# Optimization experiments

Measured on AMD Instinct MI355X. Metric: run time of the kernel, lower is better.

## Reference

```python
import jax, jax.numpy as jnp
import numpy as np

N = 100000       # nodes
E = 1600000      # edges (before self-loops)
D_IN = 128       # input feature dim
HID = 16         # hidden channels per head
HEADS = 4
D_OUT = 32       # output communities
NEG_SLOPE = 0.2  # PyG GATConv default leaky_relu slope


def setup_inputs() -> dict:
    key = jax.random.key(0)
    ks = jax.random.split(key, 10)
    s = 0.1
    x = jax.random.normal(ks[0], (N, D_IN), jnp.float32)
    edge_index = jax.random.randint(ks[1], (2, E), 0, N, dtype=jnp.int64)
    W1 = jax.random.normal(ks[2], (D_IN, HEADS * HID), jnp.float32) * s
    a_src1 = jax.random.normal(ks[3], (HEADS, HID), jnp.float32) * s
    a_dst1 = jax.random.normal(ks[4], (HEADS, HID), jnp.float32) * s
    b1 = jnp.zeros((HEADS * HID,), jnp.float32)
    W2 = jax.random.normal(ks[5], (HEADS * HID, D_OUT), jnp.float32) * s
    a_src2 = jax.random.normal(ks[6], (1, D_OUT), jnp.float32) * s
    a_dst2 = jax.random.normal(ks[7], (1, D_OUT), jnp.float32) * s
    b2 = jnp.zeros((D_OUT,), jnp.float32)
    return {"x": x, "edge_index": edge_index, "W1": W1, "a_src1": a_src1,
            "a_dst1": a_dst1, "b1": b1, "W2": W2, "a_src2": a_src2,
            "a_dst2": a_dst2, "b2": b2}


def _segment_softmax(logits, seg, n):
    # softmax over edges grouped by destination node (per head)
    m = jax.ops.segment_max(logits, seg, num_segments=n)
    m = jnp.where(jnp.isfinite(m), m, 0.0)  # guard empty segments
    e = jnp.exp(logits - m[seg])
    z = jax.ops.segment_sum(e, seg, num_segments=n)
    return e / (z[seg] + 1e-16)


def _gat_conv(x, src, dst, W, a_src, a_dst, bias, heads, out_c, concat):
    n = x.shape[0]
    h = (x @ W).reshape(n, heads, out_c)                 # [N,H,C]
    al_s = jnp.einsum('nhc,hc->nh', h, a_src)            # [N,H]
    al_d = jnp.einsum('nhc,hc->nh', h, a_dst)            # [N,H]
    logits = jax.nn.leaky_relu(al_s[src] + al_d[dst], NEG_SLOPE)  # [E,H]
    alpha = _segment_softmax(logits, dst, n)             # [E,H]
    msg = h[src] * alpha[..., None]                      # [E,H,C]
    out = jax.ops.segment_sum(msg, dst, num_segments=n)  # [N,H,C]
    out = out.reshape(n, heads * out_c) if concat else out.mean(axis=1)
    return out + bias


def reference(x, edge_index, W1, a_src1, a_dst1, b1, W2, a_src2, a_dst2, b2):
    loops = jnp.arange(N, dtype=edge_index.dtype)
    src = jnp.concatenate([edge_index[0], loops])
    dst = jnp.concatenate([edge_index[1], loops])
    h = _gat_conv(x, src, dst, W1, a_src1, a_dst1, b1, HEADS, HID, True)
    h = jax.nn.elu(h)
    return _gat_conv(h, src, dst, W2, a_src2, a_dst2, b2, 1, D_OUT, False)
```

## Files before the change

### kernel.cpp

```cpp
#include <hip/hip_runtime.h>
#include <hip/hip_fp16.h>
#include <math.h>

#define NN 100000
#define EE 1600000
#define DIN 128
#define C1 64
#define C2 32
#define NEG 0.2f

#define NB 1024
#define BSH 7
#define EPB 4096

static __device__ __forceinline__ float leaky(float x) { return x > 0.f ? x : NEG * x; }


__global__ __launch_bounds__(256) void k_chist(const int* __restrict__ ei, int* __restrict__ bhist) {
    __shared__ int h[NB];
    int t = threadIdx.x;
    for (int i = t; i < NB; i += 256) h[i] = 0;
    __syncthreads();
    int e0 = blockIdx.x * EPB;
#pragma unroll
    for (int j = 0; j < 16; j++) {
        int e = e0 + t + 256 * j;
        if (e < EE) atomicAdd(&h[ei[EE + e] >> BSH], 1);
    }
    __syncthreads();
    for (int i = t; i < NB; i += 256) {
        int c = h[i];
        if (c) atomicAdd(&bhist[i], c);
    }
}

__global__ __launch_bounds__(256) void k_bscan(const int* __restrict__ bhist,
                                               int* __restrict__ gbase, int* __restrict__ gcur) {
    __shared__ int s[256];
    int t = threadIdx.x;
    int base = t * 4;
    int v[4];
    int run = 0;
#pragma unroll
    for (int j = 0; j < 4; j++) {
        v[j] = run;
        run += bhist[base + j];
    }
    int val = run;
    s[t] = val;
    __syncthreads();
    for (int off = 1; off < 256; off <<= 1) {
        int add = (t >= off) ? s[t - off] : 0;
        __syncthreads();
        val += add;
        s[t] = val;
        __syncthreads();
    }
    int texcl = val - run;
#pragma unroll
    for (int j = 0; j < 4; j++) {
        gbase[base + j] = texcl + v[j];
        gcur[base + j] = texcl + v[j];
    }
}

__global__ __launch_bounds__(256) void k_bin(const int* __restrict__ ei, int* __restrict__ gcur,
                                             int* __restrict__ binned) {
    __shared__ int h[NB];
    __shared__ int base[NB];
    int t = threadIdx.x;
    for (int i = t; i < NB; i += 256) h[i] = 0;
    __syncthreads();
    int e0 = blockIdx.x * EPB;
    int src[16], dst[16];
#pragma unroll
    for (int j = 0; j < 16; j++) {
        int e = e0 + t + 256 * j;
        if (e < EE) {
            src[j] = ei[e];
            dst[j] = ei[EE + e];
            atomicAdd(&h[dst[j] >> BSH], 1);
        } else
            dst[j] = -1;
    }
    __syncthreads();
    for (int i = t; i < NB; i += 256) {
        int c = h[i];
        if (c) base[i] = atomicAdd(&gcur[i], c);
        h[i] = 0;
    }
    __syncthreads();
#pragma unroll
    for (int j = 0; j < 16; j++) {
        if (dst[j] >= 0) {
            int b = dst[j] >> BSH;
            int r = atomicAdd(&h[b], 1);
            binned[base[b] + r] = (src[j] << 7) | (dst[j] & 127);
        }
    }
}

__global__ __launch_bounds__(256) void k_bsort(const int* __restrict__ binned,
                                               const int* __restrict__ gbase,
                                               const int* __restrict__ bhist,
                                               int* __restrict__ rs, int* __restrict__ deg,
                                               int* __restrict__ csr) {
    __shared__ int h[128], cur[128], sc[128];
    int b = blockIdx.x, t = threadIdx.x;
    if (t < 128) h[t] = 0;
    __syncthreads();
    int gb = gbase[b], cnt = bhist[b];
    for (int i = t; i < cnt; i += 256) atomicAdd(&h[binned[gb + i] & 127], 1);
    __syncthreads();
    if (t < 128) sc[t] = h[t];
    __syncthreads();
    for (int off = 1; off < 128; off <<= 1) {
        int add = 0;
        if (t < 128 && t >= off) add = sc[t - off];
        __syncthreads();
        if (t < 128) sc[t] += add;
        __syncthreads();
    }
    if (t < 128) {
        int node = b * 128 + t;
        int excl = sc[t] - h[t];
        if (node < NN) {
            rs[node] = gb + excl;
            deg[node] = h[t];
        }
        cur[t] = excl;
    }
    __syncthreads();
    for (int i = t; i < cnt; i += 256) {
        int e = binned[gb + i];
        int r = atomicAdd(&cur[e & 127], 1);
        csr[gb + r] = e >> 7;
    }
}

__global__ __launch_bounds__(256, 2) void k_gemm1(
    const float* __restrict__ x, const float* __restrict__ W1,
    const float* __restrict__ a_s, const float* __restrict__ a_d,
    __half* __restrict__ h1h, float* __restrict__ als, float* __restrict__ ald) {
    __shared__ float xs[64 * 128];
    __shared__ float wsh[128 * 64];
    int t = threadIdx.x;
    int base = blockIdx.x * 64;
    for (int i = t; i < 2048; i += 256) ((float4*)wsh)[i] = ((const float4*)W1)[i];
    int maxn = NN - base;
    if (maxn > 64) maxn = 64;
    for (int i = t; i < 2048; i += 256) {
        int flat = i * 4;
        int n = flat >> 7;
        if (n < maxn) *(float4*)&xs[flat] = *(const float4*)&x[(size_t)(base + n) * 128 + (flat & 127)];
    }
    __syncthreads();
    int w = t >> 6, c = t & 63;
    int nb = w * 16;
    float acc[16];
#pragma unroll
    for (int j = 0; j < 16; j++) acc[j] = 0.f;
    for (int k = 0; k < 128; k += 4) {
        float w0 = wsh[k * 64 + c], w1 = wsh[(k + 1) * 64 + c];
        float w2 = wsh[(k + 2) * 64 + c], w3 = wsh[(k + 3) * 64 + c];
#pragma unroll
        for (int j = 0; j < 16; j++) {
            float4 xv = *(float4*)&xs[(nb + j) * 128 + k];
            acc[j] = fmaf(xv.x, w0, acc[j]);
            acc[j] = fmaf(xv.y, w1, acc[j]);
            acc[j] = fmaf(xv.z, w2, acc[j]);
            acc[j] = fmaf(xv.w, w3, acc[j]);
        }
    }
    float s_a = a_s[c], d_a = a_d[c];
    int hd = c >> 4;
#pragma unroll
    for (int j = 0; j < 16; j++) {
        int n = base + nb + j;
        float v = acc[j];
        float vs = v * s_a, vd = v * d_a;
#pragma unroll
        for (int off = 1; off < 16; off <<= 1) {
            vs += __shfl_xor(vs, off, 64);
            vd += __shfl_xor(vd, off, 64);
        }
        if (n < NN) {
            h1h[(size_t)n * 64 + c] = __float2half(v);
            if ((c & 15) == 0) {
                als[n * 4 + hd] = vs;
                ald[n * 4 + hd] = vd;
            }
        }
    }
}

__global__ __launch_bounds__(256) void k_edge1(
    const int* __restrict__ csr, const int* __restrict__ rs, const int* __restrict__ deg,
    const __half* __restrict__ h1h, const float* __restrict__ als, const float* __restrict__ ald,
    const float* __restrict__ b1, const float* __restrict__ W2,
    const float* __restrict__ as2, const float* __restrict__ ad2,
    __half* __restrict__ h2h, float* __restrict__ als2, float* __restrict__ ald2) {
    __shared__ float wsh[64 * 32];
    __shared__ float xld[4][64];
    __shared__ float pp[4][64][4];
    __shared__ int ss[4][64];
    int t = threadIdx.x;
    for (int i = t; i < 512; i += 256) ((float4*)wsh)[i] = ((const float4*)W2)[i];
    int w = t >> 6, lane = t & 63;
    int n = blockIdx.x * 4 + w;
    float4 ad4 = *(const float4*)&ald[n * 4];
    float4 an4 = *(const float4*)&als[n * 4];
    float ls0 = leaky(an4.x + ad4.x), ls1 = leaky(an4.y + ad4.y);
    float ls2 = leaky(an4.z + ad4.z), ls3 = leaky(an4.w + ad4.w);
    const __half2* h1p = (const __half2*)h1h;
    int cc = lane & 31, eh = lane >> 5;
    int hd2 = cc >> 3;
    float z = 0.f, acc0 = 0.f, acc1 = 0.f;
    if (eh == 0) {
        float2 fs = __half22float2(h1p[n * 32 + cc]);
        z = 1.f;
        acc0 = fs.x;
        acc1 = fs.y;
    }
    int s0 = rs[n], d = deg[n];
    for (int i0 = 0; i0 < d; i0 += 64) {
        int e = i0 + lane;
        int src = 0;
        float4 a4 = make_float4(-1e30f, -1e30f, -1e30f, -1e30f);
        if (e < d) {
            src = csr[s0 + e];
            a4 = *(const float4*)&als[src * 4];
        }
        float p0 = __expf(leaky(a4.x + ad4.x) - ls0);
        float p1 = __expf(leaky(a4.y + ad4.y) - ls1);
        float p2 = __expf(leaky(a4.z + ad4.z) - ls2);
        float p3 = __expf(leaky(a4.w + ad4.w) - ls3);
        ss[w][lane] = src;
        *(float4*)&pp[w][lane][0] = make_float4(p0, p1, p2, p3);
        int cnt = d - i0;
        if (cnt > 64) cnt = 64;
        int i = eh;
        for (; i + 6 < cnt; i += 8) {
            int sA = ss[w][i], sB = ss[w][i + 2], sC = ss[w][i + 4], sD = ss[w][i + 6];
            float pA = pp[w][i][hd2], pB = pp[w][i + 2][hd2];
            float pC = pp[w][i + 4][hd2], pD = pp[w][i + 6][hd2];
            float2 fA = __half22float2(h1p[sA * 32 + cc]);
            float2 fB = __half22float2(h1p[sB * 32 + cc]);
            float2 fC = __half22float2(h1p[sC * 32 + cc]);
            float2 fD = __half22float2(h1p[sD * 32 + cc]);
            z += (pA + pB) + (pC + pD);
            acc0 = fmaf(pA, fA.x, acc0);
            acc1 = fmaf(pA, fA.y, acc1);
            acc0 = fmaf(pB, fB.x, acc0);
            acc1 = fmaf(pB, fB.y, acc1);
            acc0 = fmaf(pC, fC.x, acc0);
            acc1 = fmaf(pC, fC.y, acc1);
            acc0 = fmaf(pD, fD.x, acc0);
            acc1 = fmaf(pD, fD.y, acc1);
        }
        for (; i < cnt; i += 2) {
            int sA = ss[w][i];
            float pA = pp[w][i][hd2];
            float2 f = __half22float2(h1p[sA * 32 + cc]);
            z += pA;
            acc0 = fmaf(pA, f.x, acc0);
            acc1 = fmaf(pA, f.y, acc1);
        }
    }
    acc0 += __shfl_xor(acc0, 32, 64);
    acc1 += __shfl_xor(acc1, 32, 64);
    z += __shfl_xor(z, 32, 64);
    float zi = __frcp_rn(z + 1e-16f);
    float o0 = acc0 * zi + b1[2 * cc];
    float o1 = acc1 * zi + b1[2 * cc + 1];
    float xv0 = o0 > 0.f ? o0 : expm1f(o0);
    float xv1 = o1 > 0.f ? o1 : expm1f(o1);
    if (eh == 0) {
        xld[w][2 * cc] = xv0;
        xld[w][2 * cc + 1] = xv1;
    }
    __syncthreads();

    int hi = lane >> 5, c2 = lane & 31;
    float accn = 0.f;
#pragma unroll
    for (int k = 0; k < 32; k++) {
        float xk = xld[w][hi * 32 + k];
        accn = fmaf(xk, wsh[(hi * 32 + k) * 32 + c2], accn);
    }
    accn += __shfl_xor(accn, 32, 64);
    float vs = accn * as2[c2], vd = accn * ad2[c2];
#pragma unroll
    for (int off = 1; off < 32; off <<= 1) {
        vs += __shfl_xor(vs, off, 64);
        vd += __shfl_xor(vd, off, 64);
    }
    if (lane < 32) h2h[(size_t)n * 32 + lane] = __float2half(accn);
    if (lane == 0) {
        als2[n] = vs;
        ald2[n] = vd;
    }
}

__global__ __launch_bounds__(256) void k_edge2(
    const int* __restrict__ csr, const int* __restrict__ rs, const int* __restrict__ deg,
    const __half* __restrict__ h2h, const float* __restrict__ als, const float* __restrict__ ald,
    const float* __restrict__ b2, float* __restrict__ out) {
    __shared__ float2 pst[4][64];
    int t = threadIdx.x;
    int w = t >> 6, lane = t & 63;
    int n = blockIdx.x * 4 + w;
    int cc = lane & 15, eq = lane >> 4;
    float ad = ald[n];
    float lself = leaky(als[n] + ad);
    const __half2* h2p = (const __half2*)h2h;
    float z = 0.f, acc0 = 0.f, acc1 = 0.f;
    if (eq == 0) {
        float2 fs = __half22float2(h2p[n * 16 + cc]);
        z = 1.f;
        acc0 = fs.x;
        acc1 = fs.y;
    }
    int s0 = rs[n], d = deg[n];
    for (int i0 = 0; i0 < d; i0 += 64) {
        int e = i0 + lane;
        int src = 0;
        float av = -1e30f;
        if (e < d) {
            src = csr[s0 + e];
            av = als[src];
        }
        float p = __expf(leaky(av + ad) - lself);
        pst[w][lane] = make_float2(__int_as_float(src), p);
        int cnt = d - i0;
        if (cnt > 64) cnt = 64;
        int i = eq;
        for (; i + 12 < cnt; i += 16) {
            float2 qA = pst[w][i], qB = pst[w][i + 4], qC = pst[w][i + 8], qD = pst[w][i + 12];
            int sA = __float_as_int(qA.x), sB = __float_as_int(qB.x);
            int sC = __float_as_int(qC.x), sD = __float_as_int(qD.x);
            float2 fA = __half22float2(h2p[sA * 16 + cc]);
            float2 fB = __half22float2(h2p[sB * 16 + cc]);
            float2 fC = __half22float2(h2p[sC * 16 + cc]);
            float2 fD = __half22float2(h2p[sD * 16 + cc]);
            z += (qA.y + qB.y) + (qC.y + qD.y);
            acc0 = fmaf(qA.y, fA.x, acc0);
            acc1 = fmaf(qA.y, fA.y, acc1);
            acc0 = fmaf(qB.y, fB.x, acc0);
            acc1 = fmaf(qB.y, fB.y, acc1);
            acc0 = fmaf(qC.y, fC.x, acc0);
            acc1 = fmaf(qC.y, fC.y, acc1);
            acc0 = fmaf(qD.y, fD.x, acc0);
            acc1 = fmaf(qD.y, fD.y, acc1);
        }
        for (; i < cnt; i += 4) {
            float2 q = pst[w][i];
            int sA = __float_as_int(q.x);
            float pA = q.y;
            float2 f = __half22float2(h2p[sA * 16 + cc]);
            z += pA;
            acc0 = fmaf(pA, f.x, acc0);
            acc1 = fmaf(pA, f.y, acc1);
        }
    }
    acc0 += __shfl_xor(acc0, 16, 64);
    acc0 += __shfl_xor(acc0, 32, 64);
    acc1 += __shfl_xor(acc1, 16, 64);
    acc1 += __shfl_xor(acc1, 32, 64);
    z += __shfl_xor(z, 16, 64);
    z += __shfl_xor(z, 32, 64);
    if (eq == 0) {
        float zi = __frcp_rn(z + 1e-16f);
        float o0 = acc0 * zi + b2[2 * cc];
        float o1 = acc1 * zi + b2[2 * cc + 1];
        *(float2*)&out[(size_t)n * 32 + 2 * cc] = make_float2(o0, o1);
    }
}

extern "C" void kernel_launch(void* const* d_in, const int* in_sizes, int n_in,
                              void* d_out, int out_size, void* d_ws, size_t ws_size,
                              hipStream_t stream) {
    const float* x = (const float*)d_in[0];
    const int* ei = (const int*)d_in[1];
    const float* W1 = (const float*)d_in[2];
    const float* as1 = (const float*)d_in[3];
    const float* ad1 = (const float*)d_in[4];
    const float* b1 = (const float*)d_in[5];
    const float* W2 = (const float*)d_in[6];
    const float* as2 = (const float*)d_in[7];
    const float* ad2 = (const float*)d_in[8];
    const float* b2 = (const float*)d_in[9];
    float* out = (float*)d_out;

    char* p = (char*)d_ws;
    auto alloc = [&](size_t bytes) -> char* {
        char* r = p;
        p += (bytes + 255) & ~(size_t)255;
        return r;
    };
    int* csr = (int*)alloc((size_t)EE * 4);
    int* rs = (int*)alloc((size_t)NN * 4);
    int* deg = (int*)alloc((size_t)NN * 4);
    int* bhist = (int*)alloc(NB * 4);
    int* gbase = (int*)alloc(NB * 4);
    int* gcur = (int*)alloc(NB * 4);
    __half* h1h = (__half*)alloc((size_t)NN * C1 * 2);
    float* als1 = (float*)alloc((size_t)NN * 4 * 4);
    float* ald1 = (float*)alloc((size_t)NN * 4 * 4);
    char* regionX = alloc((size_t)NN * C2 * 2 + (size_t)NN * 8 + 512);
    int* binned = (int*)regionX;
    __half* h2h = (__half*)regionX;
    float* als2 = (float*)(regionX + (size_t)NN * C2 * 2);
    float* ald2 = (float*)(regionX + (size_t)NN * C2 * 2 + (size_t)NN * 4);
    (void)ws_size;

    hipMemsetAsync(bhist, 0, NB * 4, stream);

    int nbin = (EE + EPB - 1) / EPB;
    k_chist<<<nbin, 256, 0, stream>>>(ei, bhist);
    k_bscan<<<1, 256, 0, stream>>>(bhist, gbase, gcur);
    k_bin<<<nbin, 256, 0, stream>>>(ei, gcur, binned);
    k_bsort<<<(NN + 127) / 128, 256, 0, stream>>>(binned, gbase, bhist, rs, deg, csr);

    k_gemm1<<<(NN + 63) / 64, 256, 0, stream>>>(x, W1, as1, ad1, h1h, als1, ald1);
    k_edge1<<<NN / 4, 256, 0, stream>>>(csr, rs, deg, h1h, als1, ald1, b1, W2, as2, ad2,
                                        h2h, als2, ald2);
    k_edge2<<<NN / 4, 256, 0, stream>>>(csr, rs, deg, h2h, als2, ald2, b2, out);
}
```

Before: 340.8 us.

## Fuse GEMM1 with histogram, vectorize edge binning, restructure edge1 LDS layout

Merges the layer-1 GEMM and the destination histogram into one launch, with extra blocks doing histogram work so the two independent stages overlap. Edge index loads in the histogram and binning kernels become int4 vector loads. k_edge1 stores per-head (src, weight) pairs in a padded LDS array, adds an 8-way unrolled gather loop, and raises the occupancy hint on both edge kernels. It also switches leaky_relu to fmaxf and ELU to __expf-1, which trades a little accuracy near zero for speed.

```diff
diff --git a/kernel.cpp b/kernel.cpp
--- a/kernel.cpp
+++ b/kernel.cpp
@@ -12,27 +12,92 @@
 #define NB 1024
 #define BSH 7
 #define EPB 4096
-
-static __device__ __forceinline__ float leaky(float x) { return x > 0.f ? x : NEG * x; }
-
-
-__global__ __launch_bounds__(256) void k_chist(const int* __restrict__ ei, int* __restrict__ bhist) {
-    __shared__ int h[NB];
+#define NGEMM 1563
+#define NCHIST 391
+
+static __device__ __forceinline__ float leaky(float x) { return fmaxf(x, NEG * x); }
+
+__global__ __launch_bounds__(256, 2) void k_gemm1_chist(
+    const float* __restrict__ x, const float* __restrict__ W1,
+    const float* __restrict__ a_s, const float* __restrict__ a_d,
+    __half* __restrict__ h1h, float* __restrict__ als, float* __restrict__ ald,
+    const int* __restrict__ ei, int* __restrict__ bhist) {
+    __shared__ float xs[64 * 128];
+    __shared__ float wsh[128 * 64];
     int t = threadIdx.x;
-    for (int i = t; i < NB; i += 256) h[i] = 0;
-    __syncthreads();
-    int e0 = blockIdx.x * EPB;
+    if (blockIdx.x >= NGEMM) {
+        int* h = (int*)xs;
+        for (int i = t; i < NB; i += 256) h[i] = 0;
+        __syncthreads();
+        const int4* d4p = (const int4*)(ei + EE);
+        int i40 = (blockIdx.x - NGEMM) * (EPB / 4);
+#pragma unroll
+        for (int j = 0; j < 4; j++) {
+            int idx = i40 + t + 256 * j;
+            if (idx < EE / 4) {
+                int4 d4 = d4p[idx];
+                atomicAdd(&h[d4.x >> BSH], 1);
+                atomicAdd(&h[d4.y >> BSH], 1);
+                atomicAdd(&h[d4.z >> BSH], 1);
+                atomicAdd(&h[d4.w >> BSH], 1);
+            }
+        }
+        __syncthreads();
+        for (int i = t; i < NB; i += 256) {
+            int c = h[i];
+            if (c) atomicAdd(&bhist[i], c);
+        }
+        return;
+    }
+    int base = blockIdx.x * 64;
+    for (int i = t; i < 2048; i += 256) ((float4*)wsh)[i] = ((const float4*)W1)[i];
+    int maxn = NN - base;
+    if (maxn > 64) maxn = 64;
+    for (int i = t; i < 2048; i += 256) {
+        int flat = i * 4;
+        int n = flat >> 7;
+        if (n < maxn) *(float4*)&xs[flat] = *(const float4*)&x[(size_t)(base + n) * 128 + (flat & 127)];
+    }
+    __syncthreads();
+    int w = t >> 6, c = t & 63;
+    int nb = w * 16;
+    float acc[16];
+#pragma unroll
+    for (int j = 0; j < 16; j++) acc[j] = 0.f;
+    for (int k = 0; k < 128; k += 4) {
+        float w0 = wsh[k * 64 + c], w1 = wsh[(k + 1) * 64 + c];
+        float w2 = wsh[(k + 2) * 64 + c], w3 = wsh[(k + 3) * 64 + c];
+#pragma unroll
+        for (int j = 0; j < 16; j++) {
+            float4 xv = *(float4*)&xs[(nb + j) * 128 + k];
+            acc[j] = fmaf(xv.x, w0, acc[j]);
+            acc[j] = fmaf(xv.y, w1, acc[j]);
+            acc[j] = fmaf(xv.z, w2, acc[j]);
+            acc[j] = fmaf(xv.w, w3, acc[j]);
+        }
+    }
+    float s_a = a_s[c], d_a = a_d[c];
+    int hd = c >> 4;
 #pragma unroll
     for (int j = 0; j < 16; j++) {
-        int e = e0 + t + 256 * j;
-        if (e < EE) atomicAdd(&h[ei[EE + e] >> BSH], 1);
-    }
-    __syncthreads();
-    for (int i = t; i < NB; i += 256) {
-        int c = h[i];
-        if (c) atomicAdd(&bhist[i], c);
-    }
-}
+        int n = base + nb + j;
+        float v = acc[j];
+        float vs = v * s_a, vd = v * d_a;
+#pragma unroll
+        for (int off = 1; off < 16; off <<= 1) {
+            vs += __shfl_xor(vs, off, 64);
+            vd += __shfl_xor(vd, off, 64);
+        }
+        if (n < NN) {
+            h1h[(size_t)n * 64 + c] = __float2half(v);
+            if ((c & 15) == 0) {
+                als[n * 4 + hd] = vs;
+                ald[n * 4 + hd] = vd;
+            }
+        }
+    }
+}
+
 
 __global__ __launch_bounds__(256) void k_bscan(const int* __restrict__ bhist,
                                                int* __restrict__ gbase, int* __restrict__ gcur) {
@@ -71,17 +136,23 @@
     int t = threadIdx.x;
     for (int i = t; i < NB; i += 256) h[i] = 0;
     __syncthreads();
-    int e0 = blockIdx.x * EPB;
-    int src[16], dst[16];
-#pragma unroll
-    for (int j = 0; j < 16; j++) {
-        int e = e0 + t + 256 * j;
-        if (e < EE) {
-            src[j] = ei[e];
-            dst[j] = ei[EE + e];
-            atomicAdd(&h[dst[j] >> BSH], 1);
-        } else
-            dst[j] = -1;
+    const int4* s4p = (const int4*)ei;
+    const int4* d4p = (const int4*)(ei + EE);
+    int i40 = blockIdx.x * (EPB / 4);
+    int4 s4[4], d4[4];
+    bool val[4];
+#pragma unroll
+    for (int j = 0; j < 4; j++) {
+        int idx = i40 + t + 256 * j;
+        val[j] = idx < EE / 4;
+        if (val[j]) {
+            s4[j] = s4p[idx];
+            d4[j] = d4p[idx];
+            atomicAdd(&h[d4[j].x >> BSH], 1);
+            atomicAdd(&h[d4[j].y >> BSH], 1);
+            atomicAdd(&h[d4[j].z >> BSH], 1);
+            atomicAdd(&h[d4[j].w >> BSH], 1);
+        }
     }
     __syncthreads();
     for (int i = t; i < NB; i += 256) {
@@ -91,11 +162,16 @@
     }
     __syncthreads();
 #pragma unroll
-    for (int j = 0; j < 16; j++) {
-        if (dst[j] >= 0) {
-            int b = dst[j] >> BSH;
-            int r = atomicAdd(&h[b], 1);
-            binned[base[b] + r] = (src[j] << 7) | (dst[j] & 127);
+    for (int j = 0; j < 4; j++) {
+        if (val[j]) {
+            int ss[4] = {s4[j].x, s4[j].y, s4[j].z, s4[j].w};
+            int dd[4] = {d4[j].x, d4[j].y, d4[j].z, d4[j].w};
+#pragma unroll
+            for (int q = 0; q < 4; q++) {
+                int b = dd[q] >> BSH;
+                int r = atomicAdd(&h[b], 1);
+                binned[base[b] + r] = (ss[q] << 7) | (dd[q] & 127);
+            }
         }
     }
 }
@@ -138,63 +214,7 @@
     }
 }
 
-__global__ __launch_bounds__(256, 2) void k_gemm1(
-    const float* __restrict__ x, const float* __restrict__ W1,
-    const float* __restrict__ a_s, const float* __restrict__ a_d,
-    __half* __restrict__ h1h, float* __restrict__ als, float* __restrict__ ald) {
-    __shared__ float xs[64 * 128];
-    __shared__ float wsh[128 * 64];
-    int t = threadIdx.x;
-    int base = blockIdx.x * 64;
-    for (int i = t; i < 2048; i += 256) ((float4*)wsh)[i] = ((const float4*)W1)[i];
-    int maxn = NN - base;
-    if (maxn > 64) maxn = 64;
-    for (int i = t; i < 2048; i += 256) {
-        int flat = i * 4;
-        int n = flat >> 7;
-        if (n < maxn) *(float4*)&xs[flat] = *(const float4*)&x[(size_t)(base + n) * 128 + (flat & 127)];
-    }
-    __syncthreads();
-    int w = t >> 6, c = t & 63;
-    int nb = w * 16;
-    float acc[16];
-#pragma unroll
-    for (int j = 0; j < 16; j++) acc[j] = 0.f;
-    for (int k = 0; k < 128; k += 4) {
-        float w0 = wsh[k * 64 + c], w1 = wsh[(k + 1) * 64 + c];
-        float w2 = wsh[(k + 2) * 64 + c], w3 = wsh[(k + 3) * 64 + c];
-#pragma unroll
-        for (int j = 0; j < 16; j++) {
-            float4 xv = *(float4*)&xs[(nb + j) * 128 + k];
-            acc[j] = fmaf(xv.x, w0, acc[j]);
-            acc[j] = fmaf(xv.y, w1, acc[j]);
-            acc[j] = fmaf(xv.z, w2, acc[j]);
-            acc[j] = fmaf(xv.w, w3, acc[j]);
-        }
-    }
-    float s_a = a_s[c], d_a = a_d[c];
-    int hd = c >> 4;
-#pragma unroll
-    for (int j = 0; j < 16; j++) {
-        int n = base + nb + j;
-        float v = acc[j];
-        float vs = v * s_a, vd = v * d_a;
-#pragma unroll
-        for (int off = 1; off < 16; off <<= 1) {
-            vs += __shfl_xor(vs, off, 64);
-            vd += __shfl_xor(vd, off, 64);
-        }
-        if (n < NN) {
-            h1h[(size_t)n * 64 + c] = __float2half(v);
-            if ((c & 15) == 0) {
-                als[n * 4 + hd] = vs;
-                ald[n * 4 + hd] = vd;
-            }
-        }
-    }
-}
-
-__global__ __launch_bounds__(256) void k_edge1(
+__global__ __launch_bounds__(256, 4) void k_edge1(
     const int* __restrict__ csr, const int* __restrict__ rs, const int* __restrict__ deg,
     const __half* __restrict__ h1h, const float* __restrict__ als, const float* __restrict__ ald,
     const float* __restrict__ b1, const float* __restrict__ W2,
@@ -202,8 +222,7 @@
     __half* __restrict__ h2h, float* __restrict__ als2, float* __restrict__ ald2) {
     __shared__ float wsh[64 * 32];
     __shared__ float xld[4][64];
-    __shared__ float pp[4][64][4];
-    __shared__ int ss[4][64];
+    __shared__ float2 epl[4][4][65];
     int t = threadIdx.x;
     for (int i = t; i < 512; i += 256) ((float4*)wsh)[i] = ((const float4*)W2)[i];
     int w = t >> 6, lane = t & 63;
@@ -231,40 +250,56 @@
             src = csr[s0 + e];
             a4 = *(const float4*)&als[src * 4];
         }
-        float p0 = __expf(leaky(a4.x + ad4.x) - ls0);
-        float p1 = __expf(leaky(a4.y + ad4.y) - ls1);
-        float p2 = __expf(leaky(a4.z + ad4.z) - ls2);
-        float p3 = __expf(leaky(a4.w + ad4.w) - ls3);
-        ss[w][lane] = src;
-        *(float4*)&pp[w][lane][0] = make_float4(p0, p1, p2, p3);
+        float fsrc = __int_as_float(src);
+        epl[w][0][lane] = make_float2(fsrc, __expf(leaky(a4.x + ad4.x) - ls0));
+        epl[w][1][lane] = make_float2(fsrc, __expf(leaky(a4.y + ad4.y) - ls1));
+        epl[w][2][lane] = make_float2(fsrc, __expf(leaky(a4.z + ad4.z) - ls2));
+        epl[w][3][lane] = make_float2(fsrc, __expf(leaky(a4.w + ad4.w) - ls3));
         int cnt = d - i0;
         if (cnt > 64) cnt = 64;
         int i = eh;
+        for (; i + 14 < cnt; i += 16) {
+            float2 q0 = epl[w][hd2][i], q1 = epl[w][hd2][i + 2];
+            float2 q2 = epl[w][hd2][i + 4], q3 = epl[w][hd2][i + 6];
+            float2 q4 = epl[w][hd2][i + 8], q5 = epl[w][hd2][i + 10];
+            float2 q6 = epl[w][hd2][i + 12], q7 = epl[w][hd2][i + 14];
+            float2 f0 = __half22float2(h1p[__float_as_int(q0.x) * 32 + cc]);
+            float2 f1 = __half22float2(h1p[__float_as_int(q1.x) * 32 + cc]);
+            float2 f2 = __half22float2(h1p[__float_as_int(q2.x) * 32 + cc]);
+            float2 f3 = __half22float2(h1p[__float_as_int(q3.x) * 32 + cc]);
+            float2 f4 = __half22float2(h1p[__float_as_int(q4.x) * 32 + cc]);
+            float2 f5 = __half22float2(h1p[__float_as_int(q5.x) * 32 + cc]);
+            float2 f6 = __half22float2(h1p[__float_as_int(q6.x) * 32 + cc]);
+            float2 f7 = __half22float2(h1p[__float_as_int(q7.x) * 32 + cc]);
+            z += ((q0.y + q1.y) + (q2.y + q3.y)) + ((q4.y + q5.y) + (q6.y + q7.y));
+            acc0 = fmaf(q0.y, f0.x, acc0); acc1 = fmaf(q0.y, f0.y, acc1);
+            acc0 = fmaf(q1.y, f1.x, acc0); acc1 = fmaf(q1.y, f1.y, acc1);
+            acc0 = fmaf(q2.y, f2.x, acc0); acc1 = fmaf(q2.y, f2.y, acc1);
+            acc0 = fmaf(q3.y, f3.x, acc0); acc1 = fmaf(q3.y, f3.y, acc1);
+            acc0 = fmaf(q4.y, f4.x, acc0); acc1 = fmaf(q4.y, f4.y, acc1);
+            acc0 = fmaf(q5.y, f5.x, acc0); acc1 = fmaf(q5.y, f5.y, acc1);
+            acc0 = fmaf(q6.y, f6.x, acc0); acc1 = fmaf(q6.y, f6.y, acc1);
+            acc0 = fmaf(q7.y, f7.x, acc0); acc1 = fmaf(q7.y, f7.y, acc1);
+        }
         for (; i + 6 < cnt; i += 8) {
-            int sA = ss[w][i], sB = ss[w][i + 2], sC = ss[w][i + 4], sD = ss[w][i + 6];
-            float pA = pp[w][i][hd2], pB = pp[w][i + 2][hd2];
-            float pC = pp[w][i + 4][hd2], pD = pp[w][i + 6][hd2];
-            float2 fA = __half22float2(h1p[sA * 32 + cc]);
-            float2 fB = __half22float2(h1p[sB * 32 + cc]);
-            float2 fC = __half22float2(h1p[sC * 32 + cc]);
-            float2 fD = __half22float2(h1p[sD * 32 + cc]);
-            z += (pA + pB) + (pC + pD);
-            acc0 = fmaf(pA, fA.x, acc0);
-            acc1 = fmaf(pA, fA.y, acc1);
-            acc0 = fmaf(pB, fB.x, acc0);
-            acc1 = fmaf(pB, fB.y, acc1);
-            acc0 = fmaf(pC, fC.x, acc0);
-            acc1 = fmaf(pC, fC.y, acc1);
-            acc0 = fmaf(pD, fD.x, acc0);
-            acc1 = fmaf(pD, fD.y, acc1);
+            float2 q0 = epl[w][hd2][i], q1 = epl[w][hd2][i + 2];
+            float2 q2 = epl[w][hd2][i + 4], q3 = epl[w][hd2][i + 6];
+            float2 f0 = __half22float2(h1p[__float_as_int(q0.x) * 32 + cc]);
+            float2 f1 = __half22float2(h1p[__float_as_int(q1.x) * 32 + cc]);
+            float2 f2 = __half22float2(h1p[__float_as_int(q2.x) * 32 + cc]);
+            float2 f3 = __half22float2(h1p[__float_as_int(q3.x) * 32 + cc]);
+            z += (q0.y + q1.y) + (q2.y + q3.y);
+            acc0 = fmaf(q0.y, f0.x, acc0); acc1 = fmaf(q0.y, f0.y, acc1);
+            acc0 = fmaf(q1.y, f1.x, acc0); acc1 = fmaf(q1.y, f1.y, acc1);
+            acc0 = fmaf(q2.y, f2.x, acc0); acc1 = fmaf(q2.y, f2.y, acc1);
+            acc0 = fmaf(q3.y, f3.x, acc0); acc1 = fmaf(q3.y, f3.y, acc1);
         }
         for (; i < cnt; i += 2) {
-            int sA = ss[w][i];
-            float pA = pp[w][i][hd2];
-            float2 f = __half22float2(h1p[sA * 32 + cc]);
-            z += pA;
-            acc0 = fmaf(pA, f.x, acc0);
-            acc1 = fmaf(pA, f.y, acc1);
+            float2 q = epl[w][hd2][i];
+            float2 f = __half22float2(h1p[__float_as_int(q.x) * 32 + cc]);
+            z += q.y;
+            acc0 = fmaf(q.y, f.x, acc0);
+            acc1 = fmaf(q.y, f.y, acc1);
         }
     }
     acc0 += __shfl_xor(acc0, 32, 64);
@@ -273,8 +308,8 @@
     float zi = __frcp_rn(z + 1e-16f);
     float o0 = acc0 * zi + b1[2 * cc];
     float o1 = acc1 * zi + b1[2 * cc + 1];
-    float xv0 = o0 > 0.f ? o0 : expm1f(o0);
-    float xv1 = o1 > 0.f ? o1 : expm1f(o1);
+    float xv0 = o0 > 0.f ? o0 : __expf(o0) - 1.f;
+    float xv1 = o1 > 0.f ? o1 : __expf(o1) - 1.f;
     if (eh == 0) {
         xld[w][2 * cc] = xv0;
         xld[w][2 * cc + 1] = xv1;
@@ -302,7 +337,7 @@
     }
 }
 
-__global__ __launch_bounds__(256) void k_edge2(
+__global__ __launch_bounds__(256, 4) void k_edge2(
     const int* __restrict__ csr, const int* __restrict__ rs, const int* __restrict__ deg,
     const __half* __restrict__ h2h, const float* __restrict__ als, const float* __restrict__ ald,
     const float* __restrict__ b2, float* __restrict__ out) {
@@ -344,14 +379,10 @@
             float2 fC = __half22float2(h2p[sC * 16 + cc]);
             float2 fD = __half22float2(h2p[sD * 16 + cc]);
             z += (qA.y + qB.y) + (qC.y + qD.y);
-            acc0 = fmaf(qA.y, fA.x, acc0);
-            acc1 = fmaf(qA.y, fA.y, acc1);
-            acc0 = fmaf(qB.y, fB.x, acc0);
-            acc1 = fmaf(qB.y, fB.y, acc1);
-            acc0 = fmaf(qC.y, fC.x, acc0);
-            acc1 = fmaf(qC.y, fC.y, acc1);
-            acc0 = fmaf(qD.y, fD.x, acc0);
-            acc1 = fmaf(qD.y, fD.y, acc1);
+            acc0 = fmaf(qA.y, fA.x, acc0); acc1 = fmaf(qA.y, fA.y, acc1);
+            acc0 = fmaf(qB.y, fB.x, acc0); acc1 = fmaf(qB.y, fB.y, acc1);
+            acc0 = fmaf(qC.y, fC.x, acc0); acc1 = fmaf(qC.y, fC.y, acc1);
+            acc0 = fmaf(qD.y, fD.x, acc0); acc1 = fmaf(qD.y, fD.y, acc1);
         }
         for (; i < cnt; i += 4) {
             float2 q = pst[w][i];
@@ -416,13 +447,12 @@
 
     hipMemsetAsync(bhist, 0, NB * 4, stream);
 
-    int nbin = (EE + EPB - 1) / EPB;
-    k_chist<<<nbin, 256, 0, stream>>>(ei, bhist);
+    k_gemm1_chist<<<NGEMM + NCHIST, 256, 0, stream>>>(x, W1, as1, ad1, h1h, als1, ald1,
+                                                      ei, bhist);
     k_bscan<<<1, 256, 0, stream>>>(bhist, gbase, gcur);
-    k_bin<<<nbin, 256, 0, stream>>>(ei, gcur, binned);
+    k_bin<<<NCHIST, 256, 0, stream>>>(ei, gcur, binned);
     k_bsort<<<(NN + 127) / 128, 256, 0, stream>>>(binned, gbase, bhist, rs, deg, csr);
 
-    k_gemm1<<<(NN + 63) / 64, 256, 0, stream>>>(x, W1, as1, ad1, h1h, als1, ald1);
     k_edge1<<<NN / 4, 256, 0, stream>>>(csr, rs, deg, h1h, als1, ald1, b1, W2, as2, ad2,
                                         h2h, als2, ald2);
     k_edge2<<<NN / 4, 256, 0, stream>>>(csr, rs, deg, h2h, als2, ald2, b2, out);
```

New measurement: 332.3 us. -2.5%, faster.
